# Kernel tuning notes

Measured on AMD Instinct MI355X. Metric: run time of the kernel, lower is better.

## Reference

```python
import jax, jax.numpy as jnp
import numpy as np

N = 50000   # nodes
E = 640000  # edges per outer layer
D = 128     # in_channels == num_hidden_channels
H = 4       # attention heads
C = D // H  # per-head dim = 32
BS = 1024   # batch_size for output slice
LN_EPS = 1e-12


def setup_inputs() -> dict:
    key = jax.random.key(0)
    ks = jax.random.split(key, 16)
    w = lambda k, shape: (jax.random.normal(k, shape, dtype=jnp.float32) * 0.05)
    return {
        "embs": jax.random.normal(ks[0], (N, D), dtype=jnp.float32),
        # GATv2 conv 0 (shared lin_l == lin_r since share_weights=True)
        "w0": w(ks[1], (D, H * C)),
        "b0": w(ks[2], (H * C,)),
        "att0": w(ks[3], (H, C)),
        "bias0": w(ks[4], (H * C,)),
        # GATv2 conv 1
        "w1": w(ks[5], (D, H * C)),
        "b1": w(ks[6], (H * C,)),
        "att1": w(ks[7], (H, C)),
        "bias1": w(ks[8], (H * C,)),
        # output head: Linear(D, D) + LayerNorm(D)
        "wout": w(ks[9], (D, D)),
        "bout": w(ks[10], (D,)),
        "gamma": jnp.ones((D,), dtype=jnp.float32),
        "beta": jnp.zeros((D,), dtype=jnp.float32),
        # graph structure (row 0 = source j, row 1 = target i, PyG convention)
        "edge_index0": jax.random.randint(ks[11], (2, E), 0, N, dtype=jnp.int32),
        "edge_index1": jax.random.randint(ks[12], (2, E), 0, N, dtype=jnp.int32),
        "batch_size": BS,
    }


def gatv2_conv(x, edge_index, w, b, att, bias):
    """PyG GATv2Conv: share_weights=True, add_self_loops=False, concat=True,
    negative_slope=0.2, edge_attr=None, eval mode (no attention dropout)."""
    xl = (x @ w + b).reshape(-1, H, C)          # [N, H, C]; x_l == x_r
    src, dst = edge_index[0], edge_index[1]
    xj = xl[src]                                # messages  [E, H, C]
    e = jax.nn.leaky_relu(xl[dst] + xj, negative_slope=0.2)
    alpha = jnp.einsum("ehc,hc->eh", e, att)    # [E, H]
    # segment softmax over incoming edges of each target node
    amax = jax.ops.segment_max(alpha, dst, num_segments=N)
    alpha = jnp.exp(alpha - amax[dst])
    denom = jax.ops.segment_sum(alpha, dst, num_segments=N)
    alpha = alpha / denom[dst]
    out = jax.ops.segment_sum(alpha[:, :, None] * xj, dst, num_segments=N)
    return out.reshape(-1, H * C) + bias        # [N, H*C]


def reference(embs, w0, b0, att0, bias0, w1, b1, att1, bias1,
              wout, bout, gamma, beta, edge_index0, edge_index1, batch_size):
    x = gatv2_conv(embs, edge_index0, w0, b0, att0, bias0)
    x = jax.nn.gelu(x, approximate=False)       # nn.GELU default (dropout is eval no-op)
    x = gatv2_conv(x, edge_index1, w1, b1, att1, bias1)
    # layernorm_output head on first batch_size nodes
    y = x[:batch_size] @ wout + bout
    mu = jnp.mean(y, axis=-1, keepdims=True)
    var = jnp.mean(jnp.square(y - mu), axis=-1, keepdims=True)
    return (y - mu) * jax.lax.rsqrt(var + LN_EPS) * gamma + beta
```

## Files before the change

kernel.cpp:

```cpp
#include <hip/hip_runtime.h>
#include <math.h>

#define DD 128
#define SLOT 64

typedef short bf16x8 __attribute__((ext_vector_type(8)));
typedef float f32x4  __attribute__((ext_vector_type(4)));

__device__ __forceinline__ unsigned bf16rne(float f) {
    unsigned u = __float_as_uint(f);
    return (u + 0x7FFFu + ((u >> 16) & 1u)) >> 16;
}
__device__ __forceinline__ float2 bf2f(unsigned u) {
    float2 r;
    r.x = __uint_as_float(u << 16);
    r.y = __uint_as_float(u & 0xFFFF0000u);
    return r;
}
__device__ __forceinline__ float gelu1(float v) {
    return 0.5f * v * (1.f + erff(v * 0.70710678118654752f));
}

struct GP {
    const float* embs;
    const float *w0, *w1, *b0, *b1;
    const float *att0, *bias0, *att1, *bias1;
    const float *wout, *bout, *gamma, *beta;
    const int *src0, *dst0, *src1, *dst1;
    unsigned* xl; float* out;
    int* ssrc; int* cnt; unsigned* mb; int* nLive; int* livelist;
    unsigned short *wp0, *wp1;
    float* yout;
    int E0, E1, N, BS, Tz, gLin, gE0, gE1;
};


__device__ __forceinline__ void mfma_lin_tile(
        const float* __restrict__ x, const bf16x8* __restrict__ wl,
        const float* __restrict__ b, unsigned* __restrict__ y,
        int tile, int nrows, int tid) {
    int wave = tid >> 6, lane = tid & 63, c = lane & 15, g = lane >> 4;
    int rb = tile * 64 + wave * 16;
    int rIn = rb + c;
    int rowValid = rIn < nrows;
    f32x4 acc[8];
    #pragma unroll
    for (int nt = 0; nt < 8; ++nt) {
        float bb = b[nt * 16 + c];
        acc[nt] = (f32x4){bb, bb, bb, bb};
    }
    for (int ks = 0; ks < 4; ++ks) {
        float xr[8];
        if (rowValid) {
            const float4* xp = (const float4*)&x[(size_t)rIn * DD + ks * 32 + g * 8];
            *(float4*)&xr[0] = xp[0];
            *(float4*)&xr[4] = xp[1];
        } else {
            #pragma unroll
            for (int j = 0; j < 8; ++j) xr[j] = 0.f;
        }
        union { unsigned u[4]; bf16x8 v; } af;
        #pragma unroll
        for (int j = 0; j < 4; ++j)
            af.u[j] = bf16rne(xr[2 * j]) | (bf16rne(xr[2 * j + 1]) << 16);
        #pragma unroll
        for (int nt = 0; nt < 8; ++nt)
            acc[nt] = __builtin_amdgcn_mfma_f32_16x16x32_bf16(
                af.v, wl[(nt * 4 + ks) * 64 + lane], acc[nt], 0, 0, 0);
    }
    int g4 = g * 4;
    #pragma unroll
    for (int nt = 0; nt < 8; ++nt) {
        #pragma unroll
        for (int reg = 0; reg < 4; ++reg) {
            unsigned u = bf16rne(acc[nt][reg]);
            unsigned up = (unsigned)__shfl_xor((int)u, 1, 64);
            int row = rb + g4 + reg;
            if (!(c & 1) && row < nrows)
                y[(size_t)row * 64 + (nt * 16 + c) / 2] = u | (up << 16);
        }
    }
}

__device__ __forceinline__ void agg_node(const unsigned* __restrict__ xl,
                                         const int* __restrict__ cnt,
                                         const int* __restrict__ ssrc,
                                         const float* __restrict__ att,
                                         const float* __restrict__ bias,
                                         int node, int key, int lane,
                                         float2* o2out) {
    float2 attv = *(const float2*)&att[lane * 2];
    float2 xd = bf2f(xl[(size_t)node * 64 + lane]);
    int rs  = key * SLOT;
    int deg = cnt[key];
    deg = deg > SLOT ? SLOT : deg;
    float m = -3.4e38f, den = 0.f, accx = 0.f, accy = 0.f;
    int sA = (deg > 0) ? ssrc[rs] : 0;
    int sB = (deg > 1) ? ssrc[rs + 1] : 0;
    unsigned uA = xl[(size_t)sA * 64 + lane];
    unsigned uB = xl[(size_t)sB * 64 + lane];
    int k = 0;
    for (; k + 1 < deg; k += 2) {
        int sC = (k + 2 < deg) ? ssrc[rs + k + 2] : 0;
        int sD = (k + 3 < deg) ? ssrc[rs + k + 3] : 0;
        unsigned uC = xl[(size_t)sC * 64 + lane];
        unsigned uD = xl[(size_t)sD * 64 + lane];
        float2 vA = bf2f(uA), vB = bf2f(uB);
        float tx = xd.x + vA.x, ty = xd.y + vA.y;
        tx = tx > 0.f ? tx : 0.2f * tx;
        ty = ty > 0.f ? ty : 0.2f * ty;
        float l0 = tx * attv.x + ty * attv.y;
        tx = xd.x + vB.x; ty = xd.y + vB.y;
        tx = tx > 0.f ? tx : 0.2f * tx;
        ty = ty > 0.f ? ty : 0.2f * ty;
        float l1 = tx * attv.x + ty * attv.y;
        #pragma unroll
        for (int o = 8; o; o >>= 1) {
            l0 += __shfl_xor(l0, o, 64);
            l1 += __shfl_xor(l1, o, 64);
        }
        float mn = fmaxf(fmaxf(m, l0), l1);
        float corr = __expf(m - mn);
        float w0 = __expf(l0 - mn);
        float w1 = __expf(l1 - mn);
        den  = den  * corr + w0 + w1;
        accx = accx * corr + w0 * vA.x + w1 * vB.x;
        accy = accy * corr + w0 * vA.y + w1 * vB.y;
        m = mn;
        sA = sC; sB = sD; uA = uC; uB = uD;
    }
    if (k < deg) {
        float2 vA = bf2f(uA);
        float tx = xd.x + vA.x, ty = xd.y + vA.y;
        tx = tx > 0.f ? tx : 0.2f * tx;
        ty = ty > 0.f ? ty : 0.2f * ty;
        float l0 = tx * attv.x + ty * attv.y;
        #pragma unroll
        for (int o = 8; o; o >>= 1) l0 += __shfl_xor(l0, o, 64);
        float mn = fmaxf(m, l0);
        float corr = __expf(m - mn);
        float w0 = __expf(l0 - mn);
        den  = den  * corr + w0;
        accx = accx * corr + w0 * vA.x;
        accy = accy * corr + w0 * vA.y;
    }
    float inv = (deg > 0) ? 1.f / den : 0.f;
    o2out->x = accx * inv + bias[lane * 2];
    o2out->y = accy * inv + bias[lane * 2 + 1];
}

__global__ __launch_bounds__(256) void k_prep(GP p) {
    int g = blockIdx.x * 256 + threadIdx.x, gs = gridDim.x * 256;
    for (int i = g; i < p.Tz; i += gs) p.cnt[i] = 0;
    for (int i = g; i < 2 * DD * DD; i += gs) {
        const float* w = (i < DD * DD) ? p.w0 : p.w1;
        unsigned short* wp = (i < DD * DD) ? p.wp0 : p.wp1;
        int q = i & (DD * DD - 1);
        int k = q >> 7, c = q & 127;
        int nt = c >> 4, ks = k >> 5;
        int lane = (c & 15) | (((k >> 3) & 3) << 4);
        wp[(((nt * 4 + ks) * 64) + lane) * 8 + (k & 7)] =
            (unsigned short)bf16rne(w[k * DD + c]);
    }
}

__global__ __launch_bounds__(256) void k_front(GP p) {
    __shared__ __align__(16) char smem[32896];
    const int tid = threadIdx.x, bid = blockIdx.x;

    if (bid < p.gE1) {
        int* lbuf = (int*)smem;
        int* lcnt = (int*)(smem + 5120);
        int* lbs  = lcnt + 1;
        if (tid == 0) *lcnt = 0;
        __syncthreads();
        int base = bid * 1024 + tid;
        #pragma unroll
        for (int j = 0; j < 4; ++j) {
            int e = base + j * 256;
            if (e < p.E1) {
                int d = p.dst1[e];
                if (d < p.BS) {
                    int s = p.src1[e];
                    int r = atomicAdd(&p.cnt[p.N + d], 1);
                    if (r < SLOT) p.ssrc[(size_t)(p.N + d) * SLOT + r] = s;
                    unsigned old = atomicOr(&p.mb[s >> 5], 1u << (s & 31));
                    if (!((old >> (s & 31)) & 1u))
                        lbuf[atomicAdd(lcnt, 1)] = s;
                }
            }
        }
        int g = bid * 256 + tid;
        if (g < p.BS) {
            unsigned old = atomicOr(&p.mb[g >> 5], 1u << (g & 31));
            if (!((old >> (g & 31)) & 1u))
                lbuf[atomicAdd(lcnt, 1)] = g;
        }
        __syncthreads();
        if (tid == 0) *lbs = atomicAdd(p.nLive, *lcnt);
        __syncthreads();
        int cN = *lcnt, bb = *lbs;
        for (int i = tid; i < cN; i += 256) p.livelist[bb + i] = lbuf[i];
        return;
    }
    if (bid < p.gE1 + p.gE0) {
        int c0 = bid - p.gE1;
        int base = c0 * 1024 + tid;
        #pragma unroll
        for (int j = 0; j < 4; ++j) {
            int e = base + j * 256;
            if (e < p.E0) {
                int d = p.dst0[e];
                int r = atomicAdd(&p.cnt[d], 1);
                if (r < SLOT) p.ssrc[(size_t)d * SLOT + r] = p.src0[e];
            }
        }
        return;
    }
    bf16x8* wl = (bf16x8*)smem;
    const bf16x8* wg = (const bf16x8*)p.wp0;
    #pragma unroll
    for (int i = 0; i < 8; ++i)
        wl[tid + i * 256] = wg[tid + i * 256];
    __syncthreads();
    mfma_lin_tile(p.embs, wl, p.b0, p.xl, bid - p.gE1 - p.gE0, p.N, tid);
}

__global__ __launch_bounds__(256) void k_aggL(GP p) {
    int li = blockIdx.x * 4 + (threadIdx.x >> 6);
    if (li >= *p.nLive) return;
    int node = __builtin_amdgcn_readfirstlane(p.livelist[li]);
    int lane = threadIdx.x & 63;
    float2 o2;
    agg_node(p.xl, p.cnt, p.ssrc, p.att0, p.bias0, node, node, lane, &o2);
    *(float2*)&p.out[(size_t)node * DD + lane * 2] = o2;
}

__global__ __launch_bounds__(256) void k_linC(GP p) {
    __shared__ bf16x8 wl[2048];
    int nL = *p.nLive;
    if (blockIdx.x * 64 >= nL) return;
    const bf16x8* wg = (const bf16x8*)p.wp1;
    #pragma unroll
    for (int i = 0; i < 8; ++i)
        wl[threadIdx.x + i * 256] = wg[threadIdx.x + i * 256];
    __syncthreads();
    int wave = threadIdx.x >> 6, lane = threadIdx.x & 63;
    int c = lane & 15, g = lane >> 4;
    int lb = blockIdx.x * 64 + wave * 16;
    int liIn = lb + c;
    int rIn = (liIn < nL) ? p.livelist[liIn] : 0;
    f32x4 acc[8];
    #pragma unroll
    for (int nt = 0; nt < 8; ++nt) {
        float bb = p.b1[nt * 16 + c];
        acc[nt] = (f32x4){bb, bb, bb, bb};
    }
    for (int ks = 0; ks < 4; ++ks) {
        float xr[8];
        if (liIn < nL) {
            const float4* xp = (const float4*)
                &p.out[(size_t)rIn * DD + ks * 32 + g * 8];
            *(float4*)&xr[0] = xp[0];
            *(float4*)&xr[4] = xp[1];
            #pragma unroll
            for (int j = 0; j < 8; ++j) xr[j] = gelu1(xr[j]);
        } else {
            #pragma unroll
            for (int j = 0; j < 8; ++j) xr[j] = 0.f;
        }
        union { unsigned u[4]; bf16x8 v; } af;
        #pragma unroll
        for (int j = 0; j < 4; ++j)
            af.u[j] = bf16rne(xr[2 * j]) | (bf16rne(xr[2 * j + 1]) << 16);
        #pragma unroll
        for (int nt = 0; nt < 8; ++nt)
            acc[nt] = __builtin_amdgcn_mfma_f32_16x16x32_bf16(
                af.v, wl[(nt * 4 + ks) * 64 + lane], acc[nt], 0, 0, 0);
    }
    int g4 = g * 4;
    #pragma unroll
    for (int reg = 0; reg < 4; ++reg) {
        int liOut = lb + g4 + reg;
        int row = (liOut < nL) ? p.livelist[liOut] : -1;
        #pragma unroll
        for (int nt = 0; nt < 8; ++nt) {
            unsigned u = bf16rne(acc[nt][reg]);
            unsigned up = (unsigned)__shfl_xor((int)u, 1, 64);
            if (!(c & 1) && row >= 0)
                p.xl[(size_t)row * 64 + (nt * 16 + c) / 2] = u | (up << 16);
        }
    }
}

__global__ __launch_bounds__(256) void k_agg1head(GP p) {
    __shared__ float xrow[4][DD];
    int wid  = threadIdx.x >> 6;
    int lane = threadIdx.x & 63;
    int node = blockIdx.x * 4 + wid;
    if (node >= p.BS) return;
    float2 o2;
    agg_node(p.xl, p.cnt, p.ssrc, p.att1, p.bias1, node, p.N + node, lane, &o2);
    xrow[wid][lane * 2]     = o2.x;
    xrow[wid][lane * 2 + 1] = o2.y;
    float2 acc2 = *(const float2*)&p.bout[lane * 2];
    __syncthreads();
    #pragma unroll 4
    for (int kk = 0; kk < DD; ++kk) {
        float xv = xrow[wid][kk];
        float2 wv2 = *(const float2*)&p.wout[(size_t)kk * DD + lane * 2];
        acc2.x += xv * wv2.x;
        acc2.y += xv * wv2.y;
    }
    float s = acc2.x + acc2.y;
    #pragma unroll
    for (int o = 32; o; o >>= 1) s += __shfl_xor(s, o, 64);
    float mean = s * (1.f / 128.f);
    float dx = acc2.x - mean, dy = acc2.y - mean;
    float s2 = dx * dx + dy * dy;
    #pragma unroll
    for (int o = 32; o; o >>= 1) s2 += __shfl_xor(s2, o, 64);
    float rstd = rsqrtf(s2 * (1.f / 128.f) + 1e-12f);
    float2 g2 = *(const float2*)&p.gamma[lane * 2];
    float2 b2 = *(const float2*)&p.beta[lane * 2];
    float2 yo;
    yo.x = dx * rstd * g2.x + b2.x;
    yo.y = dy * rstd * g2.y + b2.y;
    *(float2*)&p.yout[(size_t)node * DD + lane * 2] = yo;
}

extern "C" void kernel_launch(void* const* d_in, const int* in_sizes, int n_in,
                              void* d_out, int out_size, void* d_ws, size_t ws_size,
                              hipStream_t stream) {
    GP p;
    p.embs  = (const float*)d_in[0];
    p.w0    = (const float*)d_in[1];
    p.b0    = (const float*)d_in[2];
    p.att0  = (const float*)d_in[3];
    p.bias0 = (const float*)d_in[4];
    p.w1    = (const float*)d_in[5];
    p.b1    = (const float*)d_in[6];
    p.att1  = (const float*)d_in[7];
    p.bias1 = (const float*)d_in[8];
    p.wout  = (const float*)d_in[9];
    p.bout  = (const float*)d_in[10];
    p.gamma = (const float*)d_in[11];
    p.beta  = (const float*)d_in[12];
    const int* ei0 = (const int*)d_in[13];
    const int* ei1 = (const int*)d_in[14];

    int N  = in_sizes[0] / DD;
    int E0 = in_sizes[13] / 2;
    int E1 = in_sizes[14] / 2;
    int BS = out_size / DD;
    int n2 = N + BS;
    int W  = (N + 31) / 32;

    p.src0 = ei0;      p.dst0 = ei0 + E0;
    p.src1 = ei1;      p.dst1 = ei1 + E1;
    p.E0 = E0; p.E1 = E1; p.N = N; p.BS = BS;

    p.xl       = (unsigned*)d_ws;
    p.out      = (float*)(p.xl + (size_t)N * 64);
    p.ssrc     = (int*)(p.out + (size_t)N * DD);
    p.cnt      = p.ssrc + (size_t)n2 * SLOT;
    p.mb       = (unsigned*)(p.cnt + n2);
    p.nLive    = (int*)(p.mb + W + 32);
    p.livelist = p.nLive + 1;
    p.wp0 = (unsigned short*)
        (((uintptr_t)(p.livelist + N) + 15) & ~(uintptr_t)15);
    p.wp1 = p.wp0 + DD * DD;
    p.yout = (float*)d_out;

    p.Tz   = n2 + W + 32 + 1;
    p.gLin = (N + 63) / 64;
    p.gE0  = (E0 + 1023) / 1024;
    p.gE1  = (E1 + 1023) / 1024;

    k_prep<<<128, 256, 0, stream>>>(p);
    k_front<<<p.gE1 + p.gE0 + p.gLin, 256, 0, stream>>>(p);
    k_aggL<<<(N + 3) / 4, 256, 0, stream>>>(p);
    k_linC<<<p.gLin, 256, 0, stream>>>(p);
    k_agg1head<<<(BS + 3) / 4, 256, 0, stream>>>(p);
}
```

Measured before the change: 91.01 us.

## Split edge bucketing to fill only live-node layer-0 edges; read weights from global

The combined front kernel is split in two. One kernel marks live nodes and runs the layer-0 linear. A second kernel then buckets layer-0 edges, but only for destinations whose live bit is set, which cuts atomics and scatter writes for the many nodes not needed downstream. The MFMA weight fragments are now read directly from global memory instead of staged in LDS, dropping the shared-memory copy and barrier in exchange for repeated global/L2 reads. The split adds one extra kernel launch and serializes edge filling after marking.

```diff
diff --git a/kernel.cpp b/kernel.cpp
--- a/kernel.cpp
+++ b/kernel.cpp
@@ -34,9 +34,8 @@
     int E0, E1, N, BS, Tz, gLin, gE0, gE1;
 };
 
-
 __device__ __forceinline__ void mfma_lin_tile(
-        const float* __restrict__ x, const bf16x8* __restrict__ wl,
+        const float* __restrict__ x, const bf16x8* __restrict__ wg,
         const float* __restrict__ b, unsigned* __restrict__ y,
         int tile, int nrows, int tid) {
     int wave = tid >> 6, lane = tid & 63, c = lane & 15, g = lane >> 4;
@@ -66,7 +65,7 @@
         #pragma unroll
         for (int nt = 0; nt < 8; ++nt)
             acc[nt] = __builtin_amdgcn_mfma_f32_16x16x32_bf16(
-                af.v, wl[(nt * 4 + ks) * 64 + lane], acc[nt], 0, 0, 0);
+                af.v, wg[(nt * 4 + ks) * 64 + lane], acc[nt], 0, 0, 0);
     }
     int g4 = g * 4;
     #pragma unroll
@@ -164,15 +163,12 @@
     }
 }
 
-__global__ __launch_bounds__(256) void k_front(GP p) {
-    __shared__ __align__(16) char smem[32896];
-    const int tid = threadIdx.x, bid = blockIdx.x;
-
-    if (bid < p.gE1) {
-        int* lbuf = (int*)smem;
-        int* lcnt = (int*)(smem + 5120);
-        int* lbs  = lcnt + 1;
-        if (tid == 0) *lcnt = 0;
+__global__ __launch_bounds__(256) void k_marklin(GP p) {
+    if (blockIdx.x < p.gE1) {
+        __shared__ int lbuf[1280];
+        __shared__ int lcnt, lbase;
+        const int tid = threadIdx.x, bid = blockIdx.x;
+        if (tid == 0) lcnt = 0;
         __syncthreads();
         int base = bid * 1024 + tid;
         #pragma unroll
@@ -186,7 +182,7 @@
                     if (r < SLOT) p.ssrc[(size_t)(p.N + d) * SLOT + r] = s;
                     unsigned old = atomicOr(&p.mb[s >> 5], 1u << (s & 31));
                     if (!((old >> (s & 31)) & 1u))
-                        lbuf[atomicAdd(lcnt, 1)] = s;
+                        lbuf[atomicAdd(&lcnt, 1)] = s;
                 }
             }
         }
@@ -194,36 +190,32 @@
         if (g < p.BS) {
             unsigned old = atomicOr(&p.mb[g >> 5], 1u << (g & 31));
             if (!((old >> (g & 31)) & 1u))
-                lbuf[atomicAdd(lcnt, 1)] = g;
+                lbuf[atomicAdd(&lcnt, 1)] = g;
         }
         __syncthreads();
-        if (tid == 0) *lbs = atomicAdd(p.nLive, *lcnt);
+        if (threadIdx.x == 0) lbase = atomicAdd(p.nLive, lcnt);
         __syncthreads();
-        int cN = *lcnt, bb = *lbs;
-        for (int i = tid; i < cN; i += 256) p.livelist[bb + i] = lbuf[i];
+        for (int i = threadIdx.x; i < lcnt; i += 256)
+            p.livelist[lbase + i] = lbuf[i];
         return;
     }
-    if (bid < p.gE1 + p.gE0) {
-        int c0 = bid - p.gE1;
-        int base = c0 * 1024 + tid;
-        #pragma unroll
-        for (int j = 0; j < 4; ++j) {
-            int e = base + j * 256;
-            if (e < p.E0) {
-                int d = p.dst0[e];
+    mfma_lin_tile(p.embs, (const bf16x8*)p.wp0, p.b0, p.xl,
+                  blockIdx.x - p.gE1, p.N, threadIdx.x);
+}
+
+__global__ __launch_bounds__(256) void k_fill0(GP p) {
+    int base = blockIdx.x * 1024 + threadIdx.x;
+    #pragma unroll
+    for (int j = 0; j < 4; ++j) {
+        int e = base + j * 256;
+        if (e < p.E0) {
+            int d = p.dst0[e];
+            if ((p.mb[d >> 5] >> (d & 31)) & 1u) {
                 int r = atomicAdd(&p.cnt[d], 1);
                 if (r < SLOT) p.ssrc[(size_t)d * SLOT + r] = p.src0[e];
             }
         }
-        return;
-    }
-    bf16x8* wl = (bf16x8*)smem;
-    const bf16x8* wg = (const bf16x8*)p.wp0;
-    #pragma unroll
-    for (int i = 0; i < 8; ++i)
-        wl[tid + i * 256] = wg[tid + i * 256];
-    __syncthreads();
-    mfma_lin_tile(p.embs, wl, p.b0, p.xl, bid - p.gE1 - p.gE0, p.N, tid);
+    }
 }
 
 __global__ __launch_bounds__(256) void k_aggL(GP p) {
@@ -237,14 +229,9 @@
 }
 
 __global__ __launch_bounds__(256) void k_linC(GP p) {
-    __shared__ bf16x8 wl[2048];
     int nL = *p.nLive;
     if (blockIdx.x * 64 >= nL) return;
     const bf16x8* wg = (const bf16x8*)p.wp1;
-    #pragma unroll
-    for (int i = 0; i < 8; ++i)
-        wl[threadIdx.x + i * 256] = wg[threadIdx.x + i * 256];
-    __syncthreads();
     int wave = threadIdx.x >> 6, lane = threadIdx.x & 63;
     int c = lane & 15, g = lane >> 4;
     int lb = blockIdx.x * 64 + wave * 16;
@@ -276,7 +263,7 @@
         #pragma unroll
         for (int nt = 0; nt < 8; ++nt)
             acc[nt] = __builtin_amdgcn_mfma_f32_16x16x32_bf16(
-                af.v, wl[(nt * 4 + ks) * 64 + lane], acc[nt], 0, 0, 0);
+                af.v, wg[(nt * 4 + ks) * 64 + lane], acc[nt], 0, 0, 0);
     }
     int g4 = g * 4;
     #pragma unroll
@@ -378,8 +365,9 @@
     p.gE1  = (E1 + 1023) / 1024;
 
     k_prep<<<128, 256, 0, stream>>>(p);
-    k_front<<<p.gE1 + p.gE0 + p.gLin, 256, 0, stream>>>(p);
+    k_marklin<<<p.gE1 + p.gLin, 256, 0, stream>>>(p);
+    k_fill0<<<p.gE0, 256, 0, stream>>>(p);
     k_aggL<<<(N + 3) / 4, 256, 0, stream>>>(p);
-    k_linC<<<p.gLin, 256, 0, stream>>>(p);
+    k_linC<<<((N + 63) / 64), 256, 0, stream>>>(p);
     k_agg1head<<<(BS + 3) / 4, 256, 0, stream>>>(p);
 }
```

Result: faster. 87.18 us (-4.2%).
